# Optimization experiments

Hardware: AMD Instinct MI355X
Metric: run time of the kernel (lower is better)

The kernel has to match this reference:

```python
import jax, jax.numpy as jnp
import numpy as np

THRESHOLD1 = 1.0
THRESHOLD2 = 1.0


def _conv(x, w, stride, pad):
    return jax.lax.conv_general_dilated(
        x, w, window_strides=(stride, stride),
        padding=((pad, pad), (pad, pad)),
        dimension_numbers=('NCHW', 'OIHW', 'NCHW'))


def _percentiles_1_to_99(t):
    # Faithful to torch: k = 1 + round(0.01*q*(n-1)); kthvalue = k-th smallest.
    # One sort + static gather replaces 99 kthvalue calls.
    flat = jnp.sort(t.reshape(-1))
    n = flat.shape[0]  # static under jit
    ks = np.array([1 + round(0.01 * q * (n - 1)) for q in range(1, 100)], dtype=np.int64)
    return flat[ks - 1]  # [99]


def setup_inputs() -> dict:
    key = jax.random.key(0)
    k1, k2, k3, k4 = jax.random.split(key, 4)
    x = jax.random.normal(k1, (64, 128, 56, 56), jnp.float32)
    # Kaiming-ish scaled conv weights
    w1 = jax.random.normal(k2, (256, 128, 3, 3), jnp.float32) * (2.0 / (128 * 9)) ** 0.5
    w2 = jax.random.normal(k3, (256, 256, 3, 3), jnp.float32) * (2.0 / (256 * 9)) ** 0.5
    w_id = jax.random.normal(k4, (256, 128, 1, 1), jnp.float32) * (2.0 / 128) ** 0.5
    return {"x": x, "w1": w1, "w2": w2, "w_id": w_id}


def reference(x, w1, w2, w_id):
    out1 = _conv(x, w1, 2, 1)                 # conv1: [64,256,28,28]
    a = _percentiles_1_to_99(out1)            # percentiles of UNclamped conv1 output
    out = jnp.clip(out1, 0.0, THRESHOLD1)     # out[out>t1]=t1; out[out<0]=0
    # dropout(p=0.0 / eval) is identity
    out = _conv(out, w2, 1, 1)                # conv2
    out = out + _conv(x, w_id, 2, 0)          # residual via 1x1 stride-2 downsample
    b = _percentiles_1_to_99(out)             # percentiles before second clamp
    out = jnp.clip(out, 0.0, THRESHOLD2)
    return out, a, b
```

## Files before the change

### kernel.cpp

```cpp
#include <hip/hip_runtime.h>

typedef unsigned short ushort_t;
typedef unsigned int uint_t;

using short8 = __attribute__((ext_vector_type(8))) short;
using f32x4  = __attribute__((ext_vector_type(4))) float;

#define N_BATCH   64
#define C_MID     256
#define H_OUT     28
#define W_OUT     28
#define SPATIAL   (H_OUT*W_OUT)
#define OUT_ELEMS (N_BATCH*C_MID*SPATIAL)

#define NBINS 2048
#define BIN_LO (-16.0f)
#define BIN_INV 64.0f
#define BIN_W  0.015625f

#define XT_ROW   (57*128)
#define XT_IMG   (57*57*128)
#define O1_ROW   (30*256)
#define O1_IMG   (30*30*256)

#define WAITVM(n) asm volatile("s_waitcnt vmcnt(" #n ")" ::: "memory")
#define BARRIER() asm volatile("s_barrier" ::: "memory")

__device__ __forceinline__ ushort_t f2bf(float f) {
    uint_t u = __float_as_uint(f);
    u += 0x7FFFu + ((u >> 16) & 1u);
    return (ushort_t)(u >> 16);
}

__device__ __forceinline__ void gll16(const ushort_t* g, void* l) {
    __builtin_amdgcn_global_load_lds(
        (const __attribute__((address_space(1))) unsigned int*)g,
        (__attribute__((address_space(3))) unsigned int*)l, 16, 0, 0);
}

__global__ __launch_bounds__(256) void zwtrans(
    uint_t* __restrict__ xT32, uint_t* __restrict__ o1T32,
    const float* __restrict__ w1, const float* __restrict__ w2,
    const float* __restrict__ wid, ushort_t* __restrict__ wT1,
    ushort_t* __restrict__ wT2)
{
    const int bxx = blockIdx.x, y = blockIdx.y, tid = threadIdx.x;
    if (bxx < 87) {
        int i = bxx * 256 + tid;
        int n = y;
        if (i >= 22080) return;
        if (i < 7232) {
            uint_t* base = xT32 + (size_t)n * (XT_IMG / 2);
            if (i < 3648) base[i] = 0;
            else { int j = i - 3648; int r = (j >> 6) + 1;
                   base[r * (XT_ROW / 2) + (j & 63)] = 0; }
        } else {
            int k = i - 7232;
            uint_t* base = o1T32 + (size_t)n * (O1_IMG / 2);
            if (k < 3840) base[k] = 0;
            else if (k < 7680) base[29 * (O1_ROW / 2) + (k - 3840)] = 0;
            else if (k < 11264) { int j = k - 7680; int r = (j >> 7) + 1;
                   base[r * (O1_ROW / 2) + (j & 127)] = 0; }
            else { int j = k - 11264; int r = (j >> 7) + 1;
                   base[r * (O1_ROW / 2) + 29 * 128 + (j & 127)] = 0; }
        }
    } else {
        int idx = ((bxx - 87) * 64 + y) * 256 + tid;
        if (idx < 256 * 1152) {
            int co = idx / 1152, k = idx % 1152;
            int g = k >> 7, ci = k & 127;
            wT1[idx] = f2bf(w1[(co * 128 + ci) * 9 + g]);
        }
        if (idx < 256 * 2432) {
            int co = idx / 2432, k = idx % 2432;
            float v;
            if (k < 2304) { int g = k >> 8, ci = k & 255; v = w2[(co * 256 + ci) * 9 + g]; }
            else          { v = wid[co * 128 + (k - 2304)]; }
            wT2[idx] = f2bf(v);
        }
    }
}

__global__ __launch_bounds__(256) void xtrans(
    const float* __restrict__ x, ushort_t* __restrict__ xT)
{
    __shared__ ushort_t t[224 * 130];
    const int tid = threadIdx.x;
    const int g = blockIdx.x, n = blockIdx.y;
    const float* xs = x + ((size_t)n * 128) * 3136 + g * 4 * 56;

    for (int it = 0; it < 112; ++it) {
        int f = it * 256 + tid;
        int ci = f / 224, rem = f % 224;
        t[rem * 130 + ci] = f2bf(xs[ci * 3136 + rem]);
    }
    __syncthreads();
    ushort_t* xo = xT + (size_t)n * XT_IMG + (g * 4 + 1) * XT_ROW + 128;
    for (int it = 0; it < 56; ++it) {
        int f = it * 256 + tid;
        int pos = f >> 6, c2 = f & 63;
        int r = pos / 56, iw = pos % 56;
        uint_t v = *(const uint_t*)&t[pos * 130 + c2 * 2];
        *(uint_t*)(xo + r * XT_ROW + iw * 128 + c2 * 2) = v;
    }
}

__global__ __launch_bounds__(256, 2) void conv1_mfma(
    const ushort_t* __restrict__ xT, const ushort_t* __restrict__ wT1,
    ushort_t* __restrict__ o1T, ushort_t* __restrict__ bh)
{
    const int bx = blockIdx.x;
    const int tid = threadIdx.x;
    const int wv = tid >> 6, lane = tid & 63;
    const int ln = lane & 15, quad = lane >> 4;
    const int n = bx / 7, rg = bx % 7, r0 = rg * 4;

    __shared__ short8 Ald[2 * 1024];
    __shared__ short8 Bp[2304];

    f32x4 acc[4][7];
    #pragma unroll
    for (int a = 0; a < 4; ++a)
        #pragma unroll
        for (int b = 0; b < 7; ++b) acc[a][b] = (f32x4){0.f, 0.f, 0.f, 0.f};

    int drb[7], cl0[7];
    #pragma unroll
    for (int b = 0; b < 7; ++b) {
        int p = b * 16 + ln;
        drb[b] = 2 * (p / 28);
        cl0[b] = p % 28;
    }

    uint_t poff[9];
    #pragma unroll
    for (int i = 0; i < 9; ++i) {
        int slot = (i * 4 + wv) * 64 + lane;
        int s2 = min(slot, 2051);
        int k8 = s2 / 513;
        int rem = s2 - k8 * 513;
        int dr = rem / 57, j = rem - dr * 57;
        int col = (j < 29) ? (2 * j) : (2 * (j - 29) + 1);
        poff[i] = (uint_t)((2 * r0 + dr) * XT_ROW + col * 128 + k8 * 8);
    }
    const uint_t aoff = (uint_t)((wv * 64 + lane) * 1152);

    const ushort_t* xTimg = xT + (size_t)n * XT_IMG;

    auto stageA = [&](int tap, int c, int buf) {
        #pragma unroll
        for (int jj = 0; jj < 4; ++jj)
            gll16(wT1 + aoff + jj * 8 + tap * 128 + c * 32,
                  (char*)Ald + buf * 16384 + (jj * 256 + wv * 64) * 16);
    };

    for (int c = 0; c < 4; ++c) {
        BARRIER();
        #pragma unroll
        for (int i = 0; i < 9; ++i)
            gll16(xTimg + poff[i] + c * 32, (char*)Bp + ((i * 4 + wv) * 64) * 16);
        if (c == 0) stageA(0, 0, 0);
        WAITVM(0);
        BARRIER();

        #pragma unroll
        for (int t = 0; t < 9; ++t) {
            const int st = c * 9 + t;
            const int buf = st & 1;
            if (t < 8)      stageA(t + 1, c, buf ^ 1);
            else if (c < 3) stageA(0, c + 1, buf ^ 1);
            if (c == 3 && t == 8) { WAITVM(0); } else { WAITVM(4); }
            const int kh = t / 3, kw = t - kh * 3;
            short8 af[4], bf[7];
            #pragma unroll
            for (int a = 0; a < 4; ++a)
                af[a] = Ald[buf * 1024 + quad * 256 + wv * 64 + a * 16 + ln];
            #pragma unroll
            for (int b = 0; b < 7; ++b) {
                int dr = drb[b] + kh;
                int j = (kw == 1) ? (29 + cl0[b]) : (cl0[b] + (kw >> 1));
                bf[b] = Bp[quad * 513 + dr * 57 + j];
            }
            __builtin_amdgcn_s_setprio(1);
            #pragma unroll
            for (int a = 0; a < 4; ++a)
                #pragma unroll
                for (int b = 0; b < 7; ++b)
                    acc[a][b] = __builtin_amdgcn_mfma_f32_16x16x32_bf16(
                        af[a], bf[b], acc[a][b], 0, 0, 0);
            __builtin_amdgcn_s_setprio(0);
        }
    }

    __syncthreads();
    uint_t* hist = (uint_t*)Ald;
    for (int i = tid; i < NBINS; i += 256) hist[i] = 0;
    __syncthreads();

    ushort_t* oimg = o1T + (size_t)n * O1_IMG;
    #pragma unroll
    for (int a = 0; a < 4; ++a) {
        int co = wv * 64 + a * 16 + quad * 4;
        #pragma unroll
        for (int b = 0; b < 7; ++b) {
            int p = b * 16 + ln;
            int h = r0 + p / 28, w = p % 28;
            ushort_t pk[4];
            #pragma unroll
            for (int r = 0; r < 4; ++r) {
                float v = acc[a][b][r];
                int bin = (int)((v - BIN_LO) * BIN_INV);
                bin = min(max(bin, 0), NBINS - 1);
                atomicAdd(&hist[bin], 1u);
                pk[r] = f2bf(fminf(fmaxf(v, 0.f), 1.f));
            }
            uint2 u; u.x = (uint_t)pk[0] | ((uint_t)pk[1] << 16);
            u.y = (uint_t)pk[2] | ((uint_t)pk[3] << 16);
            *(uint2*)(oimg + ((h + 1) * 30 + (w + 1)) * 256 + co) = u;
        }
    }

    __syncthreads();
    size_t blin = (size_t)bx * NBINS;
    for (int i = tid; i < NBINS; i += 256) bh[blin + i] = (ushort_t)hist[i];
}

__global__ __launch_bounds__(256, 2) void conv2_mfma(
    const ushort_t* __restrict__ o1T, const ushort_t* __restrict__ xT,
    const ushort_t* __restrict__ wT2, float* __restrict__ fout,
    ushort_t* __restrict__ bh)
{
    const int bx = blockIdx.x;
    const int by = blockIdx.y;
    const int tid = threadIdx.x;
    const int wv = tid >> 6, lane = tid & 63;
    const int ln = lane & 15, quad = lane >> 4;
    const int n = bx >> 2, rg = bx & 3, r0 = rg * 8;
    const int coh = wv & 1;
    const int pt  = wv >> 1;

    __shared__ short8 Ad[3 * 512];
    __shared__ short8 Bp[2 * 1280];

    f32x4 acc[4][7];
    #pragma unroll
    for (int a = 0; a < 4; ++a)
        #pragma unroll
        for (int b = 0; b < 7; ++b) acc[a][b] = (f32x4){0.f, 0.f, 0.f, 0.f};

    int prb[7], cl0[7], hlog[7];
    #pragma unroll
    for (int b = 0; b < 7; ++b) {
        int p = b * 16 + ln;
        int h = r0 + pt * 4 + p / 28;
        hlog[b] = h;
        prb[b] = (min(h, 27) - r0) * 32;
        cl0[b] = p % 28;
    }

    uint_t po[5];
    #pragma unroll
    for (int jj = 0; jj < 5; ++jj) {
        int f = (wv * 5 + jj) * 64 + lane;
        int ci8 = f / 320, rem = f % 320;
        int dr = rem >> 5, cl = rem & 31;
        po[jj] = (uint_t)(min(r0 + dr, 29) * O1_ROW + cl * 256 + ci8 * 8);
    }
    uint_t io[4];
    #pragma unroll
    for (int jj = 0; jj < 4; ++jj) {
        int i2 = min(wv * 4 + jj, 13);
        int slot = i2 * 64 + lane;
        int ci8 = slot / 224, pos = slot % 224;
        int h = min(r0 + pos / 28, 27), w = pos % 28;
        io[jj] = (uint_t)(((2 * h + 1) * 57 + (2 * w + 1)) * 128 + ci8 * 8);
    }

    const ushort_t* o1img = o1T + (size_t)n * O1_IMG;
    const ushort_t* xTimg = xT + (size_t)n * XT_IMG;
    const ushort_t* Ab0 = wT2 + (size_t)(by * 128 + lane) * 2432 + wv * 8;
    const ushort_t* Ab1 = Ab0 + (size_t)64 * 2432;

    auto stageA = [&](int k0, int buf) {
        gll16(Ab0 + k0, (char*)Ad + buf * 8192 + wv * 2048);
        gll16(Ab1 + k0, (char*)Ad + buf * 8192 + wv * 2048 + 1024);
    };
    auto stageB = [&](int hb, int coff) {
        #pragma unroll
        for (int jj = 0; jj < 5; ++jj)
            gll16(o1img + po[jj] + coff, (char*)Bp + hb * 20480 + (wv * 5 + jj) * 1024);
    };
    auto stageI = [&](int ib, int idh) {
        #pragma unroll
        for (int jj = 0; jj < 4; ++jj) {
            int i2 = min(wv * 4 + jj, 13);
            gll16(xTimg + io[jj] + idh * 32, (char*)Bp + ib * 20480 + i2 * 1024);
        }
    };

    stageB(0, 0);
    stageA(0, 0);

    for (int h = 0; h < 8; ++h) {
        #pragma unroll
        for (int t = 0; t < 9; ++t) {
            if (t < 8)      stageA((t + 1) * 256 + h * 32, (t + 1) % 3);
            else if (h < 7) stageA((h + 1) * 32, 0);
            else            stageA(2304, 0);
            if (t == 1) {
                if (h < 7) { stageB((h + 1) & 1, (h + 1) * 32); WAITVM(7); }
                else       { stageI(0, 0);                      WAITVM(6); }
            } else {
                WAITVM(2);
            }
            BARRIER();
            const int abuf = t % 3;
            const int kh = t / 3, kw = t - kh * 3;
            short8 af[4], bf[7];
            #pragma unroll
            for (int a = 0; a < 4; ++a)
                af[a] = Ad[abuf * 512 + quad * 128 + coh * 64 + a * 16 + ln];
            #pragma unroll
            for (int b = 0; b < 7; ++b)
                bf[b] = Bp[(h & 1) * 1280 + quad * 320 + prb[b] + kh * 32 + cl0[b] + kw];
            __builtin_amdgcn_s_setprio(1);
            #pragma unroll
            for (int a = 0; a < 4; ++a)
                #pragma unroll
                for (int b = 0; b < 7; ++b)
                    acc[a][b] = __builtin_amdgcn_mfma_f32_16x16x32_bf16(
                        af[a], bf[b], acc[a][b], 0, 0, 0);
            __builtin_amdgcn_s_setprio(0);
        }
    }

    #pragma unroll
    for (int idh = 0; idh < 4; ++idh) {
        if (idh < 3) { stageA(2304 + (idh + 1) * 32, (idh + 1) % 3); WAITVM(2); }
        else         { WAITVM(0); }
        BARRIER();
        if (idh < 3) stageI((idh + 1) & 1, idh + 1);
        short8 af[4], bf[7];
        #pragma unroll
        for (int a = 0; a < 4; ++a)
            af[a] = Ad[(idh % 3) * 512 + quad * 128 + coh * 64 + a * 16 + ln];
        #pragma unroll
        for (int b = 0; b < 7; ++b)
            bf[b] = Bp[(idh & 1) * 1280 + quad * 224 + pt * 112 + b * 16 + ln];
        __builtin_amdgcn_s_setprio(1);
        #pragma unroll
        for (int a = 0; a < 4; ++a)
            #pragma unroll
            for (int b = 0; b < 7; ++b)
                acc[a][b] = __builtin_amdgcn_mfma_f32_16x16x32_bf16(
                    af[a], bf[b], acc[a][b], 0, 0, 0);
        __builtin_amdgcn_s_setprio(0);
    }

    __syncthreads();
    uint_t* hist = (uint_t*)Ad;
    for (int i = tid; i < NBINS; i += 256) hist[i] = 0;
    __syncthreads();

    #pragma unroll
    for (int a = 0; a < 4; ++a) {
        int co = by * 128 + coh * 64 + a * 16 + quad * 4;
        #pragma unroll
        for (int b = 0; b < 7; ++b) {
            if (hlog[b] <= 27) {
                #pragma unroll
                for (int r = 0; r < 4; ++r) {
                    float v = acc[a][b][r];
                    int bin = (int)((v - BIN_LO) * BIN_INV);
                    bin = min(max(bin, 0), NBINS - 1);
                    atomicAdd(&hist[bin], 1u);
                    fout[((size_t)(n * 256 + co + r)) * SPATIAL +
                         hlog[b] * 28 + cl0[b]] = fminf(fmaxf(v, 0.f), 1.f);
                }
            }
        }
    }

    __syncthreads();
    size_t blin = (size_t)(by * 256 + bx) * NBINS;
    for (int i = tid; i < NBINS; i += 256) bh[blin + i] = (ushort_t)hist[i];
}

__global__ __launch_bounds__(256) void hreduce(
    const ushort_t* __restrict__ bh, uint_t* __restrict__ hf, int nblk)
{
    __shared__ uint_t p[256];
    int b0 = blockIdx.x * 64;
    int binl = threadIdx.x & 63, grp = threadIdx.x >> 6;
    uint_t s = 0;
    for (int j = grp; j < nblk; j += 4) s += bh[(size_t)j * NBINS + b0 + binl];
    p[threadIdx.x] = s;
    __syncthreads();
    if (threadIdx.x < 64)
        hf[b0 + threadIdx.x] = p[threadIdx.x] + p[64 + threadIdx.x] +
                               p[128 + threadIdx.x] + p[192 + threadIdx.x];
}

__global__ __launch_bounds__(1024) void select_k(
    const uint_t* __restrict__ hf, float* __restrict__ outp)
{
    __shared__ uint_t cs[1024];
    int t = threadIdx.x;
    uint_t s = hf[2 * t] + hf[2 * t + 1];
    cs[t] = s;
    __syncthreads();
    for (int d = 1; d < 1024; d <<= 1) {
        uint_t v = (t >= d) ? cs[t - d] : 0;
        __syncthreads();
        cs[t] += v;
        __syncthreads();
    }
    if (t >= 1 && t <= 99) {
        long long k = 1 + (long long)llrint(0.01 * (double)t * (double)(OUT_ELEMS - 1));
        int lo = 0, hi = 1023;
        while (lo < hi) { int mid = (lo + hi) >> 1; if ((long long)cs[mid] < k) lo = mid + 1; else hi = mid; }
        long long cum = (lo == 0) ? 0 : (long long)cs[lo - 1];
        int b = lo * 2;
        while (cum + (long long)hf[b] < k) { cum += hf[b]; ++b; }
        outp[t - 1] = BIN_LO + ((float)b + 0.5f) * BIN_W;
    }
}

extern "C" void kernel_launch(void* const* d_in, const int* in_sizes, int n_in,
                              void* d_out, int out_size, void* d_ws, size_t ws_size,
                              hipStream_t stream)
{
    const float* x   = (const float*)d_in[0];
    const float* w1  = (const float*)d_in[1];
    const float* w2  = (const float*)d_in[2];
    const float* wid = (const float*)d_in[3];
    float* out = (float*)d_out;

    char* ws = (char*)d_ws;
    ushort_t* xT  = (ushort_t*)ws;
    ushort_t* o1T = (ushort_t*)(ws + 53235712);
    ushort_t* wT1 = (ushort_t*)(ws + 82731008);
    ushort_t* wT2 = (ushort_t*)(ws + 83320832);
    ushort_t* bhA = (ushort_t*)(ws + 84566016);
    ushort_t* bhB = (ushort_t*)(ws + 86401024);
    uint_t*   hfA = (uint_t*)  (ws + 88498176);
    uint_t*   hfB = (uint_t*)  (ws + 88506368);

    zwtrans<<<dim3(125, 64), 256, 0, stream>>>((uint_t*)xT, (uint_t*)o1T,
                                               w1, w2, wid, wT1, wT2);
    xtrans<<<dim3(14, 64), 256, 0, stream>>>(x, xT);

    conv1_mfma<<<448, 256, 0, stream>>>(xT, wT1, o1T, bhA);
    conv2_mfma<<<dim3(256, 2), 256, 0, stream>>>(o1T, xT, wT2, out, bhB);

    hreduce<<<32, 256, 0, stream>>>(bhA, hfA, 448);
    select_k<<<1, 1024, 0, stream>>>(hfA, out + OUT_ELEMS);
    hreduce<<<32, 256, 0, stream>>>(bhB, hfB, 512);
    select_k<<<1, 1024, 0, stream>>>(hfB, out + OUT_ELEMS + 99);
}
```

Before: 393.4 us.

## Give each wave private double-buffered weight tiles to drop per-step barriers in conv2

New measurement: 419.7 us. 6.7% more time.

```diff
diff --git a/kernel.cpp b/kernel.cpp
--- a/kernel.cpp
+++ b/kernel.cpp
@@ -239,7 +239,7 @@
     const int coh = wv & 1;
     const int pt  = wv >> 1;
 
-    __shared__ short8 Ad[3 * 512];
+    __shared__ short8 Ad[2 * 1024];
     __shared__ short8 Bp[2 * 1280];
 
     f32x4 acc[4][7];
@@ -278,12 +278,13 @@
 
     const ushort_t* o1img = o1T + (size_t)n * O1_IMG;
     const ushort_t* xTimg = xT + (size_t)n * XT_IMG;
-    const ushort_t* Ab0 = wT2 + (size_t)(by * 128 + lane) * 2432 + wv * 8;
-    const ushort_t* Ab1 = Ab0 + (size_t)64 * 2432;
-
-    auto stageA = [&](int k0, int buf) {
-        gll16(Ab0 + k0, (char*)Ad + buf * 8192 + wv * 2048);
-        gll16(Ab1 + k0, (char*)Ad + buf * 8192 + wv * 2048 + 1024);
+    const ushort_t* wAsrc = wT2 + (size_t)(by * 128 + coh * 64 + lane) * 2432;
+
+    auto stageA4 = [&](int k0, int buf) {
+        #pragma unroll
+        for (int j = 0; j < 4; ++j)
+            gll16(wAsrc + k0 + j * 8,
+                  (char*)Ad + buf * 16384 + wv * 4096 + j * 1024);
     };
     auto stageB = [&](int hb, int coff) {
         #pragma unroll
@@ -299,27 +300,30 @@
     };
 
     stageB(0, 0);
-    stageA(0, 0);
+    stageA4(0, 0);
+    WAITVM(0);
+    BARRIER();
 
     for (int h = 0; h < 8; ++h) {
+        if (h) BARRIER();
         #pragma unroll
         for (int t = 0; t < 9; ++t) {
-            if (t < 8)      stageA((t + 1) * 256 + h * 32, (t + 1) % 3);
-            else if (h < 7) stageA((h + 1) * 32, 0);
-            else            stageA(2304, 0);
+            const int rb = (h * 9 + t) & 1, wb = rb ^ 1;
+            if (t < 8) stageA4((t + 1) * 256 + h * 32, wb);
+            else       stageA4((h < 7) ? (h + 1) * 32 : 2304, wb);
             if (t == 1) {
-                if (h < 7) { stageB((h + 1) & 1, (h + 1) * 32); WAITVM(7); }
-                else       { stageI(0, 0);                      WAITVM(6); }
+                if (h < 7) { stageB((h + 1) & 1, (h + 1) * 32); WAITVM(9); }
+                else       { stageI(0, 0);                      WAITVM(8); }
+            } else if (t == 2) {
+                if (h < 7) { WAITVM(9); } else { WAITVM(8); }
             } else {
-                WAITVM(2);
+                WAITVM(4);
             }
-            BARRIER();
-            const int abuf = t % 3;
             const int kh = t / 3, kw = t - kh * 3;
             short8 af[4], bf[7];
             #pragma unroll
             for (int a = 0; a < 4; ++a)
-                af[a] = Ad[abuf * 512 + quad * 128 + coh * 64 + a * 16 + ln];
+                af[a] = Ad[rb * 1024 + wv * 256 + quad * 64 + a * 16 + ln];
             #pragma unroll
             for (int b = 0; b < 7; ++b)
                 bf[b] = Bp[(h & 1) * 1280 + quad * 320 + prb[b] + kh * 32 + cl0[b] + kw];
@@ -336,14 +340,16 @@
 
     #pragma unroll
     for (int idh = 0; idh < 4; ++idh) {
-        if (idh < 3) { stageA(2304 + (idh + 1) * 32, (idh + 1) % 3); WAITVM(2); }
-        else         { WAITVM(0); }
+        WAITVM(0);
         BARRIER();
-        if (idh < 3) stageI((idh + 1) & 1, idh + 1);
+        if (idh < 3) {
+            stageA4(2304 + (idh + 1) * 32, (idh + 1) & 1);
+            stageI((idh + 1) & 1, idh + 1);
+        }
         short8 af[4], bf[7];
         #pragma unroll
         for (int a = 0; a < 4; ++a)
-            af[a] = Ad[(idh % 3) * 512 + quad * 128 + coh * 64 + a * 16 + ln];
+            af[a] = Ad[(idh & 1) * 1024 + wv * 256 + quad * 64 + a * 16 + ln];
         #pragma unroll
         for (int b = 0; b < 7; ++b)
             bf[b] = Bp[(idh & 1) * 1280 + quad * 224 + pt * 112 + b * 16 + ln];
```

## Widen conv kernels to 512 threads and retile conv2 to full-channel 4-row blocks

Applied to the files above, without the earlier changes.

Result: slower. 431.3 us (+9.6%).

```diff
diff --git a/kernel.cpp b/kernel.cpp
--- a/kernel.cpp
+++ b/kernel.cpp
@@ -105,7 +105,7 @@
     }
 }
 
-__global__ __launch_bounds__(256, 2) void conv1_mfma(
+__global__ __launch_bounds__(512, 4) void conv1_mfma(
     const ushort_t* __restrict__ xT, const ushort_t* __restrict__ wT1,
     ushort_t* __restrict__ o1T, ushort_t* __restrict__ bh)
 {
@@ -118,9 +118,9 @@
     __shared__ short8 Ald[2 * 1024];
     __shared__ short8 Bp[2304];
 
-    f32x4 acc[4][7];
-    #pragma unroll
-    for (int a = 0; a < 4; ++a)
+    f32x4 acc[2][7];
+    #pragma unroll
+    for (int a = 0; a < 2; ++a)
         #pragma unroll
         for (int b = 0; b < 7; ++b) acc[a][b] = (f32x4){0.f, 0.f, 0.f, 0.f};
 
@@ -132,10 +132,11 @@
         cl0[b] = p % 28;
     }
 
-    uint_t poff[9];
-    #pragma unroll
-    for (int i = 0; i < 9; ++i) {
-        int slot = (i * 4 + wv) * 64 + lane;
+    uint_t poff[5];
+    #pragma unroll
+    for (int i = 0; i < 5; ++i) {
+        int it = i * 8 + wv;
+        int slot = it * 64 + lane;
         int s2 = min(slot, 2051);
         int k8 = s2 / 513;
         int rem = s2 - k8 * 513;
@@ -143,38 +144,46 @@
         int col = (j < 29) ? (2 * j) : (2 * (j - 29) + 1);
         poff[i] = (uint_t)((2 * r0 + dr) * XT_ROW + col * 128 + k8 * 8);
     }
-    const uint_t aoff = (uint_t)((wv * 64 + lane) * 1152);
+    const ushort_t* asrc[2];
+    #pragma unroll
+    for (int jj = 0; jj < 2; ++jj) {
+        int elem = jj * 64 + lane;
+        int k8e = elem >> 5, cor = elem & 31;
+        asrc[jj] = wT1 + (size_t)(wv * 32 + cor) * 1152 + k8e * 8;
+    }
 
     const ushort_t* xTimg = xT + (size_t)n * XT_IMG;
 
     auto stageA = [&](int tap, int c, int buf) {
         #pragma unroll
-        for (int jj = 0; jj < 4; ++jj)
-            gll16(wT1 + aoff + jj * 8 + tap * 128 + c * 32,
-                  (char*)Ald + buf * 16384 + (jj * 256 + wv * 64) * 16);
+        for (int jj = 0; jj < 2; ++jj)
+            gll16(asrc[jj] + tap * 128 + c * 32,
+                  (char*)Ald + buf * 16384 + wv * 2048 + jj * 1024);
     };
 
     for (int c = 0; c < 4; ++c) {
         BARRIER();
         #pragma unroll
-        for (int i = 0; i < 9; ++i)
-            gll16(xTimg + poff[i] + c * 32, (char*)Bp + ((i * 4 + wv) * 64) * 16);
+        for (int i = 0; i < 5; ++i) {
+            int it = i * 8 + wv;
+            if (it < 36)
+                gll16(xTimg + poff[i] + c * 32, (char*)Bp + it * 1024);
+        }
         if (c == 0) stageA(0, 0, 0);
         WAITVM(0);
         BARRIER();
 
-        #pragma unroll
         for (int t = 0; t < 9; ++t) {
             const int st = c * 9 + t;
             const int buf = st & 1;
             if (t < 8)      stageA(t + 1, c, buf ^ 1);
             else if (c < 3) stageA(0, c + 1, buf ^ 1);
-            if (c == 3 && t == 8) { WAITVM(0); } else { WAITVM(4); }
+            if (c == 3 && t == 8) { WAITVM(0); } else { WAITVM(2); }
             const int kh = t / 3, kw = t - kh * 3;
-            short8 af[4], bf[7];
-            #pragma unroll
-            for (int a = 0; a < 4; ++a)
-                af[a] = Ald[buf * 1024 + quad * 256 + wv * 64 + a * 16 + ln];
+            short8 af[2], bf[7];
+            #pragma unroll
+            for (int a = 0; a < 2; ++a)
+                af[a] = Ald[buf * 1024 + wv * 128 + quad * 32 + a * 16 + ln];
             #pragma unroll
             for (int b = 0; b < 7; ++b) {
                 int dr = drb[b] + kh;
@@ -183,7 +192,7 @@
             }
             __builtin_amdgcn_s_setprio(1);
             #pragma unroll
-            for (int a = 0; a < 4; ++a)
+            for (int a = 0; a < 2; ++a)
                 #pragma unroll
                 for (int b = 0; b < 7; ++b)
                     acc[a][b] = __builtin_amdgcn_mfma_f32_16x16x32_bf16(
@@ -194,13 +203,13 @@
 
     __syncthreads();
     uint_t* hist = (uint_t*)Ald;
-    for (int i = tid; i < NBINS; i += 256) hist[i] = 0;
+    for (int i = tid; i < NBINS; i += 512) hist[i] = 0;
     __syncthreads();
 
     ushort_t* oimg = o1T + (size_t)n * O1_IMG;
     #pragma unroll
-    for (int a = 0; a < 4; ++a) {
-        int co = wv * 64 + a * 16 + quad * 4;
+    for (int a = 0; a < 2; ++a) {
+        int co = wv * 32 + a * 16 + quad * 4;
         #pragma unroll
         for (int b = 0; b < 7; ++b) {
             int p = b * 16 + ln;
@@ -222,29 +231,26 @@
 
     __syncthreads();
     size_t blin = (size_t)bx * NBINS;
-    for (int i = tid; i < NBINS; i += 256) bh[blin + i] = (ushort_t)hist[i];
-}
-
-__global__ __launch_bounds__(256, 2) void conv2_mfma(
+    for (int i = tid; i < NBINS; i += 512) bh[blin + i] = (ushort_t)hist[i];
+}
+
+__global__ __launch_bounds__(512, 4) void conv2_mfma(
     const ushort_t* __restrict__ o1T, const ushort_t* __restrict__ xT,
     const ushort_t* __restrict__ wT2, float* __restrict__ fout,
     ushort_t* __restrict__ bh)
 {
     const int bx = blockIdx.x;
-    const int by = blockIdx.y;
     const int tid = threadIdx.x;
     const int wv = tid >> 6, lane = tid & 63;
     const int ln = lane & 15, quad = lane >> 4;
-    const int n = bx >> 2, rg = bx & 3, r0 = rg * 8;
-    const int coh = wv & 1;
-    const int pt  = wv >> 1;
-
-    __shared__ short8 Ad[3 * 512];
-    __shared__ short8 Bp[2 * 1280];
-
-    f32x4 acc[4][7];
-    #pragma unroll
-    for (int a = 0; a < 4; ++a)
+    const int n = bx / 7, rg = bx % 7, r0 = rg * 4;
+
+    __shared__ short8 Ad[3 * 1024];
+    __shared__ short8 Bp[2 * 768];
+
+    f32x4 acc[2][7];
+    #pragma unroll
+    for (int a = 0; a < 2; ++a)
         #pragma unroll
         for (int b = 0; b < 7; ++b) acc[a][b] = (f32x4){0.f, 0.f, 0.f, 0.f};
 
@@ -252,54 +258,61 @@
     #pragma unroll
     for (int b = 0; b < 7; ++b) {
         int p = b * 16 + ln;
-        int h = r0 + pt * 4 + p / 28;
-        hlog[b] = h;
-        prb[b] = (min(h, 27) - r0) * 32;
+        int hl = p / 28;
+        hlog[b] = r0 + hl;
+        prb[b] = hl * 32;
         cl0[b] = p % 28;
     }
 
-    uint_t po[5];
-    #pragma unroll
-    for (int jj = 0; jj < 5; ++jj) {
-        int f = (wv * 5 + jj) * 64 + lane;
-        int ci8 = f / 320, rem = f % 320;
+    uint_t po[2];
+    #pragma unroll
+    for (int jj = 0; jj < 2; ++jj) {
+        int i2 = min(wv * 2 + jj, 11);
+        int f = i2 * 64 + lane;
+        int ci8 = f / 192, rem = f % 192;
         int dr = rem >> 5, cl = rem & 31;
-        po[jj] = (uint_t)(min(r0 + dr, 29) * O1_ROW + cl * 256 + ci8 * 8);
-    }
-    uint_t io[4];
-    #pragma unroll
-    for (int jj = 0; jj < 4; ++jj) {
-        int i2 = min(wv * 4 + jj, 13);
-        int slot = i2 * 64 + lane;
-        int ci8 = slot / 224, pos = slot % 224;
-        int h = min(r0 + pos / 28, 27), w = pos % 28;
-        io[jj] = (uint_t)(((2 * h + 1) * 57 + (2 * w + 1)) * 128 + ci8 * 8);
+        po[jj] = (uint_t)((r0 + dr) * O1_ROW + cl * 256 + ci8 * 8);
+    }
+    uint_t io;
+    int islot;
+    {
+        islot = min(wv, 6);
+        int f = islot * 64 + lane;
+        int ci8 = f / 112, pos = f % 112;
+        int h = r0 + pos / 28, w = pos % 28;
+        io = (uint_t)(((2 * h + 1) * 57 + (2 * w + 1)) * 128 + ci8 * 8);
+    }
+    const ushort_t* asrc[2];
+    int adst[2];
+    #pragma unroll
+    for (int jj = 0; jj < 2; ++jj) {
+        int i = wv * 2 + jj;
+        asrc[jj] = wT2 + (size_t)((i & 3) * 64 + lane) * 2432 + (i >> 2) * 8;
+        adst[jj] = i * 1024;
     }
 
     const ushort_t* o1img = o1T + (size_t)n * O1_IMG;
     const ushort_t* xTimg = xT + (size_t)n * XT_IMG;
-    const ushort_t* Ab0 = wT2 + (size_t)(by * 128 + lane) * 2432 + wv * 8;
-    const ushort_t* Ab1 = Ab0 + (size_t)64 * 2432;
 
     auto stageA = [&](int k0, int buf) {
-        gll16(Ab0 + k0, (char*)Ad + buf * 8192 + wv * 2048);
-        gll16(Ab1 + k0, (char*)Ad + buf * 8192 + wv * 2048 + 1024);
+        #pragma unroll
+        for (int jj = 0; jj < 2; ++jj)
+            gll16(asrc[jj] + k0, (char*)Ad + buf * 16384 + adst[jj]);
     };
     auto stageB = [&](int hb, int coff) {
         #pragma unroll
-        for (int jj = 0; jj < 5; ++jj)
-            gll16(o1img + po[jj] + coff, (char*)Bp + hb * 20480 + (wv * 5 + jj) * 1024);
+        for (int jj = 0; jj < 2; ++jj)
+            gll16(o1img + po[jj] + coff,
+                  (char*)Bp + hb * 12288 + min(wv * 2 + jj, 11) * 1024);
     };
     auto stageI = [&](int ib, int idh) {
-        #pragma unroll
-        for (int jj = 0; jj < 4; ++jj) {
-            int i2 = min(wv * 4 + jj, 13);
-            gll16(xTimg + io[jj] + idh * 32, (char*)Bp + ib * 20480 + i2 * 1024);
-        }
+        gll16(xTimg + io + idh * 32, (char*)Bp + ib * 12288 + islot * 1024);
     };
 
     stageB(0, 0);
     stageA(0, 0);
+    WAITVM(0);
+    BARRIER();
 
     for (int h = 0; h < 8; ++h) {
         #pragma unroll
@@ -308,24 +321,26 @@
             else if (h < 7) stageA((h + 1) * 32, 0);
             else            stageA(2304, 0);
             if (t == 1) {
-                if (h < 7) { stageB((h + 1) & 1, (h + 1) * 32); WAITVM(7); }
-                else       { stageI(0, 0);                      WAITVM(6); }
+                if (h < 7) { stageB((h + 1) & 1, (h + 1) * 32); WAITVM(4); }
+                else       { stageI(0, 0);                      WAITVM(3); }
+            } else if (t == 2) {
+                if (h < 7) { WAITVM(4); } else { WAITVM(3); }
             } else {
                 WAITVM(2);
             }
             BARRIER();
-            const int abuf = t % 3;
+            const int ab = t % 3;
             const int kh = t / 3, kw = t - kh * 3;
-            short8 af[4], bf[7];
-            #pragma unroll
-            for (int a = 0; a < 4; ++a)
-                af[a] = Ad[abuf * 512 + quad * 128 + coh * 64 + a * 16 + ln];
+            short8 af[2], bf[7];
+            #pragma unroll
+            for (int a = 0; a < 2; ++a)
+                af[a] = Ad[ab * 1024 + quad * 256 + wv * 32 + a * 16 + ln];
             #pragma unroll
             for (int b = 0; b < 7; ++b)
-                bf[b] = Bp[(h & 1) * 1280 + quad * 320 + prb[b] + kh * 32 + cl0[b] + kw];
+                bf[b] = Bp[(h & 1) * 768 + quad * 192 + prb[b] + kh * 32 + cl0[b] + kw];
             __builtin_amdgcn_s_setprio(1);
             #pragma unroll
-            for (int a = 0; a < 4; ++a)
+            for (int a = 0; a < 2; ++a)
                 #pragma unroll
                 for (int b = 0; b < 7; ++b)
                     acc[a][b] = __builtin_amdgcn_mfma_f32_16x16x32_bf16(
@@ -336,20 +351,22 @@
 
     #pragma unroll
     for (int idh = 0; idh < 4; ++idh) {
-        if (idh < 3) { stageA(2304 + (idh + 1) * 32, (idh + 1) % 3); WAITVM(2); }
-        else         { WAITVM(0); }
+        WAITVM(0);
         BARRIER();
-        if (idh < 3) stageI((idh + 1) & 1, idh + 1);
-        short8 af[4], bf[7];
-        #pragma unroll
-        for (int a = 0; a < 4; ++a)
-            af[a] = Ad[(idh % 3) * 512 + quad * 128 + coh * 64 + a * 16 + ln];
+        if (idh < 3) {
+            stageA(2304 + (idh + 1) * 32, (idh + 1) % 3);
+            stageI((idh + 1) & 1, idh + 1);
+        }
+        short8 af[2], bf[7];
+        #pragma unroll
+        for (int a = 0; a < 2; ++a)
+            af[a] = Ad[(idh % 3) * 1024 + quad * 256 + wv * 32 + a * 16 + ln];
         #pragma unroll
         for (int b = 0; b < 7; ++b)
-            bf[b] = Bp[(idh & 1) * 1280 + quad * 224 + pt * 112 + b * 16 + ln];
+            bf[b] = Bp[(idh & 1) * 768 + quad * 112 + b * 16 + ln];
         __builtin_amdgcn_s_setprio(1);
         #pragma unroll
-        for (int a = 0; a < 4; ++a)
+        for (int a = 0; a < 2; ++a)
             #pragma unroll
             for (int b = 0; b < 7; ++b)
                 acc[a][b] = __builtin_amdgcn_mfma_f32_16x16x32_bf16(
@@ -359,31 +376,29 @@
 
     __syncthreads();
     uint_t* hist = (uint_t*)Ad;
-    for (int i = tid; i < NBINS; i += 256) hist[i] = 0;
-    __syncthreads();
-
-    #pragma unroll
-    for (int a = 0; a < 4; ++a) {
-        int co = by * 128 + coh * 64 + a * 16 + quad * 4;
+    for (int i = tid; i < NBINS; i += 512) hist[i] = 0;
+    __syncthreads();
+
+    #pragma unroll
+    for (int a = 0; a < 2; ++a) {
+        int co = wv * 32 + a * 16 + quad * 4;
         #pragma unroll
         for (int b = 0; b < 7; ++b) {
-            if (hlog[b] <= 27) {
-                #pragma unroll
-                for (int r = 0; r < 4; ++r) {
-                    float v = acc[a][b][r];
-                    int bin = (int)((v - BIN_LO) * BIN_INV);
-                    bin = min(max(bin, 0), NBINS - 1);
-                    atomicAdd(&hist[bin], 1u);
-                    fout[((size_t)(n * 256 + co + r)) * SPATIAL +
-                         hlog[b] * 28 + cl0[b]] = fminf(fmaxf(v, 0.f), 1.f);
-                }
+            #pragma unroll
+            for (int r = 0; r < 4; ++r) {
+                float v = acc[a][b][r];
+                int bin = (int)((v - BIN_LO) * BIN_INV);
+                bin = min(max(bin, 0), NBINS - 1);
+                atomicAdd(&hist[bin], 1u);
+                fout[((size_t)(n * 256 + co + r)) * SPATIAL +
+                     hlog[b] * 28 + cl0[b]] = fminf(fmaxf(v, 0.f), 1.f);
             }
         }
     }
 
     __syncthreads();
-    size_t blin = (size_t)(by * 256 + bx) * NBINS;
-    for (int i = tid; i < NBINS; i += 256) bh[blin + i] = (ushort_t)hist[i];
+    size_t blin = (size_t)bx * NBINS;
+    for (int i = tid; i < NBINS; i += 512) bh[blin + i] = (ushort_t)hist[i];
 }
 
 __global__ __launch_bounds__(256) void hreduce(
@@ -450,11 +465,11 @@
                                                w1, w2, wid, wT1, wT2);
     xtrans<<<dim3(14, 64), 256, 0, stream>>>(x, xT);
 
-    conv1_mfma<<<448, 256, 0, stream>>>(xT, wT1, o1T, bhA);
-    conv2_mfma<<<dim3(256, 2), 256, 0, stream>>>(o1T, xT, wT2, out, bhB);
+    conv1_mfma<<<448, 512, 0, stream>>>(xT, wT1, o1T, bhA);
+    conv2_mfma<<<448, 512, 0, stream>>>(o1T, xT, wT2, out, bhB);
 
     hreduce<<<32, 256, 0, stream>>>(bhA, hfA, 448);
     select_k<<<1, 1024, 0, stream>>>(hfA, out + OUT_ELEMS);
-    hreduce<<<32, 256, 0, stream>>>(bhB, hfB, 512);
+    hreduce<<<32, 256, 0, stream>>>(bhB, hfB, 448);
     select_k<<<1, 1024, 0, stream>>>(hfB, out + OUT_ELEMS + 99);
 }
```
